# Kernel optimization log

Measured on AMD Instinct MI355X. Metric: run time of the kernel, lower is better.

The kernel has to match this reference:

```python
import jax, jax.numpy as jnp
import numpy as np

NH = 8    # num_heads
HD = 64   # head_dim
EPS = 1e-6


def setup_inputs() -> dict:
    key = jax.random.key(0)
    ks = jax.random.split(key, 8)
    B, N, D = 16, 3136, 512
    x = jax.random.normal(ks[0], (B, N, D), jnp.float32)
    Wq = jax.random.normal(ks[1], (D, D), jnp.float32) * 0.02
    Wkv = jax.random.normal(ks[2], (D, 2 * D), jnp.float32) * 0.02
    pos_enc = jax.random.normal(ks[3], (1, N, D), jnp.float32) * 0.02
    # depthwise conv: fan_out = k*k*out/groups = 25
    dwc_w = jax.random.normal(ks[4], (HD, 1, 5, 5), jnp.float32) * np.sqrt(2.0 / 25.0).astype(np.float32)
    dwc_b = jnp.zeros((HD,), jnp.float32)
    Wp = jax.random.normal(ks[5], (D, D), jnp.float32) * 0.02
    bp = jnp.zeros((D,), jnp.float32)
    return {"x": x, "Wq": Wq, "Wkv": Wkv, "pos_enc": pos_enc,
            "dwc_w": dwc_w, "dwc_b": dwc_b, "Wp": Wp, "bp": bp,
            "H": 56, "W": 56}


def reference(x, Wq, Wkv, pos_enc, dwc_w, dwc_b, Wp, bp, H, W):
    B, N, D = x.shape
    # projections (qkv_bias=False)
    q = jax.nn.relu(x @ Wq)                       # ReLU feature map on q
    kv = x @ Wkv                                  # [B, N, 2D]
    k = jax.nn.relu(kv[..., :D] + pos_enc)        # pos enc added before ReLU kernel
    v = kv[..., D:]
    # split heads: b n (h c) -> b h n c
    qh = q.reshape(B, N, NH, HD).transpose(0, 2, 1, 3)
    kh = k.reshape(B, N, NH, HD).transpose(0, 2, 1, 3)
    vh = v.reshape(B, N, NH, HD).transpose(0, 2, 1, 3)
    # linear attention: normalization and KV context
    k_sum = kh.sum(axis=2)                                        # [B, NH, HD]
    d_inv = 1.0 / (jnp.einsum('bhnd,bhd->bhn', qh, k_sum) + EPS)  # [B, NH, N]
    ctx = jnp.einsum('bhmd,bhme->bhde', kh, vh)                   # [B, NH, HD, HD]
    attn = jnp.einsum('bhnd,bhde->bhne', qh, ctx) * d_inv[..., None]
    # depthwise conv positional mixing on v (N == H*W)
    fmap = vh.reshape(B * NH, H, W, HD).transpose(0, 3, 1, 2)     # [(b h), c, H, W]
    dwc = jax.lax.conv_general_dilated(
        fmap, dwc_w, window_strides=(1, 1), padding='SAME',
        feature_group_count=HD,
        dimension_numbers=('NCHW', 'OIHW', 'NCHW')) + dwc_b[None, :, None, None]
    dwc = dwc.transpose(0, 2, 3, 1).reshape(B, NH, N, HD)
    # NOTE: original torch code reshapes ((b h), n, c) -> (B, N, D) directly
    # (NOT the inverse rearrange); reproduce that exact flat reshape.
    out = (attn + dwc).reshape(B, N, D)
    return out @ Wp + bp
```

## Files before the change

### kernel.cpp

```cpp
#include <hip/hip_runtime.h>

__device__ __forceinline__ float b2f(ushort u) {
    union { float f; unsigned int i; } w; w.i = ((unsigned int)u) << 16; return w.f;
}
__device__ __forceinline__ ushort f2b(float f) {
    union { float f; unsigned int i; } w; w.f = f;
    unsigned int lsb = (w.i >> 16) & 1u;
    w.i += 0x7fffu + lsb;
    return (ushort)(w.i >> 16);
}

typedef __bf16 bf16x8 __attribute__((ext_vector_type(8)));
typedef float floatx4 __attribute__((ext_vector_type(4)));

__device__ __forceinline__ void async_copy16(ushort* lds_base, const ushort* gptr) {
    __builtin_amdgcn_global_load_lds(
        (const __attribute__((address_space(1))) unsigned int*)gptr,
        (__attribute__((address_space(3))) unsigned int*)lds_base,
        16, 0, 0);
}

#define BATCH 16
#define NTOK  3136
#define NHEAD 8
#define HDIM  64
#define HSP   56
#define MROWS (BATCH * NTOK)
#define KDIM  512

__global__ __launch_bounds__(256) void detect_dtype(const ushort* __restrict__ x,
                                                    int* __restrict__ flag)
{
    __shared__ int s;
    if (threadIdx.x == 0) s = 0;
    __syncthreads();
    int bad = 0;
    for (int i = threadIdx.x; i < 4096; i += 256) {
        int e = (x[i] >> 7) & 0xFF;
        if (e >= 0x90) bad = 1;
    }
    if (bad) s = 1;
    __syncthreads();
    if (threadIdx.x == 0) flag[0] = s;
}

__global__ __launch_bounds__(256) void convert_x(
    const void* __restrict__ x, const int* __restrict__ flag,
    ushort* __restrict__ xbf)
{
    size_t t = (size_t)blockIdx.x * 256 + threadIdx.x;
    if (flag[0]) {
        const float* xf = (const float*)x + t * 8;
        float4 f0 = *(const float4*)xf;
        float4 f1 = *(const float4*)(xf + 4);
        ushort o[8] = { f2b(f0.x), f2b(f0.y), f2b(f0.z), f2b(f0.w),
                        f2b(f1.x), f2b(f1.y), f2b(f1.z), f2b(f1.w) };
        *(uint4*)(xbf + t * 8) = *(const uint4*)o;
    } else {
        *(uint4*)(xbf + t * 8) = *((const uint4*)x + t);
    }
}

__global__ __launch_bounds__(256) void prep_weights(
    const void* __restrict__ Wq, const void* __restrict__ Wkv,
    const void* __restrict__ Wp, const int* __restrict__ flag,
    ushort* __restrict__ WqkvT, ushort* __restrict__ WpT)
{
    bool f32 = flag[0] != 0;
    int idx = blockIdx.x * 256 + threadIdx.x;
    int kk = idx & 511;
    int n  = idx >> 9;
    if (n < 1536) {
        ushort val;
        if (n < 512)
            val = f32 ? f2b(((const float*)Wq)[kk * 512 + n])
                      : ((const ushort*)Wq)[kk * 512 + n];
        else
            val = f32 ? f2b(((const float*)Wkv)[kk * 1024 + (n - 512)])
                      : ((const ushort*)Wkv)[kk * 1024 + (n - 512)];
        WqkvT[n * 512 + kk] = val;
    } else {
        int n2 = n - 1536;
        WpT[n2 * 512 + kk] = f32 ? f2b(((const float*)Wp)[kk * 512 + n2])
                                 : ((const ushort*)Wp)[kk * 512 + n2];
    }
}

__global__ __launch_bounds__(256) void prep_dwc(
    const void* __restrict__ dwc_w, const void* __restrict__ dwc_b,
    const int* __restrict__ flag, float* __restrict__ wT)
{
    bool f32 = flag[0] != 0;
    for (int i = threadIdx.x; i < 1600; i += 256) {
        int e = i / 25, tap = i % 25;
        float w = f32 ? ((const float*)dwc_w)[i] : b2f(((const ushort*)dwc_w)[i]);
        wT[tap * 64 + e] = w;
    }
    if (threadIdx.x < 64) {
        float b = f32 ? ((const float*)dwc_b)[threadIdx.x]
                      : b2f(((const ushort*)dwc_b)[threadIdx.x]);
        wT[1600 + threadIdx.x] = b;
    }
}

__device__ __forceinline__ int swz(int r) { return (r ^ (r >> 2)) & 3; }

#define VMWAIT(N) asm volatile("s_waitcnt vmcnt(" #N ")" ::: "memory")
#define LGKM0()   do { asm volatile("s_waitcnt lgkmcnt(0)" ::: "memory"); \
                       __builtin_amdgcn_sched_barrier(0); } while (0)
#define ASLOT(u,h) ((((u) & 1) * 2 + (h)) * 8192)
#define BSLOT(u,h) (32768 + (((u) & 1) * 2 + (h)) * 8192)

__global__ __launch_bounds__(512, 2) void gemm256_bt(
    const ushort* __restrict__ A, const ushort* __restrict__ Bt,
    int mode, const int* __restrict__ flag,
    const void* __restrict__ pos_enc, const void* __restrict__ bias,
    void* __restrict__ out0, ushort* __restrict__ out1, ushort* __restrict__ out2,
    int ntn)
{
    __shared__ ushort smem[65536];

    const bool f32 = flag[0] != 0;
    const int tid = threadIdx.x;
    const int lam = tid & 63;
    const int w   = tid >> 6;
    const int wm  = w >> 2;
    const int wn  = w & 3;
    const int g    = lam >> 4;
    const int mrow = lam & 15;

    const int nwg = gridDim.x;
    const int q8  = nwg >> 3;
    const int bid = blockIdx.x;
    const int fid = (bid & 7) * q8 + (bid >> 3);
    const int tm = fid / ntn, tn = fid - tm * ntn;
    const int m0 = tm * 256, n0 = tn * 256;

    const int srow  = w * 16 + (lam >> 3);
    const int scol8 = 8 * ((lam & 7) ^ (lam >> 3));
    const ushort* gA0 = A  + (size_t)(m0 +       srow) * KDIM + scol8;
    const ushort* gA1 = A  + (size_t)(m0 + 128 + srow) * KDIM + scol8;
    const ushort* gB0 = Bt + (size_t)(n0 +       srow) * KDIM + scol8;
    const ushort* gB1 = Bt + (size_t)(n0 + 128 + srow) * KDIM + scol8;

    const int m7  = mrow & 7;
    const int kx0 = 8 * (g ^ m7);
    const int kx1 = 8 * ((4 + g) ^ m7);
    const int aRow = mrow * 64;
    const int bRow = ((wn & 1) * 64 + mrow) * 64;

    floatx4 acc[8][4];
    #pragma unroll
    for (int i = 0; i < 8; i++)
        #pragma unroll
        for (int j = 0; j < 4; j++) acc[i][j] = (floatx4)0.f;

#define STG(gp, sb, ko) do { \
    async_copy16(smem + (sb) + w * 1024,       (gp) + (ko)); \
    async_copy16(smem + (sb) + w * 1024 + 512, (gp) + 4096 + (ko)); } while (0)

    STG(gA0, ASLOT(0,0), 0);  STG(gA1, ASLOT(0,1), 0);
    STG(gB0, BSLOT(0,0), 0);  STG(gB1, BSLOT(0,1), 0);
    STG(gA0, ASLOT(1,0), 64); STG(gA1, ASLOT(1,1), 64);
    STG(gB0, BSLOT(1,0), 64); STG(gB1, BSLOT(1,1), 64);
    VMWAIT(8);
    __builtin_amdgcn_s_barrier();

    bf16x8 a[2][2], bb[4][2];

#define PHASE_MFMA(P) do { \
    __builtin_amdgcn_s_setprio(1); \
    _Pragma("unroll") \
    for (int q = 0; q < 2; ++q) \
        _Pragma("unroll") \
        for (int fc = 0; fc < 4; ++fc) { \
            acc[2*(P)+q][fc] = __builtin_amdgcn_mfma_f32_16x16x32_bf16( \
                bb[fc][0], a[q][0], acc[2*(P)+q][fc], 0, 0, 0); \
            acc[2*(P)+q][fc] = __builtin_amdgcn_mfma_f32_16x16x32_bf16( \
                bb[fc][1], a[q][1], acc[2*(P)+q][fc], 0, 0, 0); \
        } \
    __builtin_amdgcn_s_setprio(0); } while (0)

    #pragma unroll
    for (int u = 0; u < 8; ++u) {
        const ushort* sa = smem + ASLOT(u, wm) + aRow;
        const ushort* sb = smem + BSLOT(u, (wn >> 1)) + bRow;

        #pragma unroll
        for (int q = 0; q < 2; ++q) {
            a[q][0] = *(const bf16x8*)(sa + q * 1024 + kx0);
            a[q][1] = *(const bf16x8*)(sa + q * 1024 + kx1);
        }
        #pragma unroll
        for (int fc = 0; fc < 4; ++fc) {
            bb[fc][0] = *(const bf16x8*)(sb + fc * 1024 + kx0);
            bb[fc][1] = *(const bf16x8*)(sb + fc * 1024 + kx1);
        }
        if (u >= 1 && u <= 6) STG(gA0, ASLOT(u + 1, 0), (u + 1) * 64);
        __builtin_amdgcn_s_barrier();
        LGKM0();
        PHASE_MFMA(0);
        __builtin_amdgcn_s_barrier();

        #pragma unroll
        for (int q = 0; q < 2; ++q) {
            a[q][0] = *(const bf16x8*)(sa + (2 + q) * 1024 + kx0);
            a[q][1] = *(const bf16x8*)(sa + (2 + q) * 1024 + kx1);
        }
        if (u >= 1 && u <= 6) STG(gA1, ASLOT(u + 1, 1), (u + 1) * 64);
        if (u <= 5)           STG(gB0, BSLOT(u + 2, 0), (u + 2) * 64);
        __builtin_amdgcn_s_barrier();
        LGKM0();
        PHASE_MFMA(1);
        __builtin_amdgcn_s_barrier();

        #pragma unroll
        for (int q = 0; q < 2; ++q) {
            a[q][0] = *(const bf16x8*)(sa + (4 + q) * 1024 + kx0);
            a[q][1] = *(const bf16x8*)(sa + (4 + q) * 1024 + kx1);
        }
        if (u <= 5) STG(gB1, BSLOT(u + 2, 1), (u + 2) * 64);
        __builtin_amdgcn_s_barrier();
        LGKM0();
        PHASE_MFMA(2);
        __builtin_amdgcn_s_barrier();

        #pragma unroll
        for (int q = 0; q < 2; ++q) {
            a[q][0] = *(const bf16x8*)(sa + (6 + q) * 1024 + kx0);
            a[q][1] = *(const bf16x8*)(sa + (6 + q) * 1024 + kx1);
        }
        __builtin_amdgcn_s_barrier();
        LGKM0();
        PHASE_MFMA(3);
        if (u <= 5)      VMWAIT(4);
        else if (u == 6) VMWAIT(0);
        if (u < 7) __builtin_amdgcn_s_barrier();
    }

    const int cb0 = n0 + wn * 64;
    #pragma unroll
    for (int fr = 0; fr < 8; ++fr) {
        const int rg  = m0 + wm * 128 + fr * 16 + mrow;
        const int bb2 = rg / NTOK;
        const int nn  = rg - bb2 * NTOK;
        if (mode == 1) {
            if (f32) {
                float* orow = (float*)out0 + (size_t)rg * 512 + cb0 + g * 4;
                #pragma unroll
                for (int fc = 0; fc < 4; ++fc) {
                    float ob[4];
                    #pragma unroll
                    for (int r = 0; r < 4; ++r)
                        ob[r] = acc[fr][fc][r] +
                                ((const float*)bias)[cb0 + fc * 16 + g * 4 + r];
                    *(float4*)(orow + fc * 16) = *(const float4*)ob;
                }
            } else {
                ushort* orow = (ushort*)out0 + (size_t)rg * 512 + cb0 + g * 4;
                #pragma unroll
                for (int fc = 0; fc < 4; ++fc) {
                    ushort t4[4];
                    #pragma unroll
                    for (int r = 0; r < 4; ++r)
                        t4[r] = f2b(acc[fr][fc][r] +
                                    b2f(((const ushort*)bias)[cb0 + fc * 16 + g * 4 + r]));
                    *(uint2*)(orow + fc * 16) = *(const uint2*)t4;
                }
            }
        } else {
            const int tz   = cb0 >> 9;
            const int head = (cb0 >> 6) & 7;
            const size_t obase =
                (((size_t)bb2 * 8 + head) * NTOK + nn) * 64 + g * 4;
            if (tz == 0) {
                #pragma unroll
                for (int fc = 0; fc < 4; ++fc) {
                    ushort t4[4];
                    #pragma unroll
                    for (int r = 0; r < 4; ++r)
                        t4[r] = f2b(fmaxf(acc[fr][fc][r], 0.f));
                    *(uint2*)((ushort*)out0 + obase + fc * 16) = *(const uint2*)t4;
                }
            } else if (tz == 1) {
                const int d0 = cb0 - 512 + g * 4;
                #pragma unroll
                for (int fc = 0; fc < 4; ++fc) {
                    ushort t4[4];
                    #pragma unroll
                    for (int r = 0; r < 4; ++r) {
                        float pe = f32
                            ? ((const float*)pos_enc)[(size_t)nn * 512 + d0 + fc * 16 + r]
                            : b2f(((const ushort*)pos_enc)[(size_t)nn * 512 + d0 + fc * 16 + r]);
                        t4[r] = f2b(fmaxf(acc[fr][fc][r] + pe, 0.f));
                    }
                    *(uint2*)(out1 + obase + fc * 16) = *(const uint2*)t4;
                }
            } else {
                #pragma unroll
                for (int fc = 0; fc < 4; ++fc) {
                    ushort t4[4];
                    #pragma unroll
                    for (int r = 0; r < 4; ++r)
                        t4[r] = f2b(acc[fr][fc][r]);
                    *(uint2*)(out2 + obase + fc * 16) = *(const uint2*)t4;
                }
            }
        }
    }
#undef STG
#undef PHASE_MFMA
}

#define SPLITS 7
#define NPER   (NTOK / SPLITS)

__global__ __launch_bounds__(256) void ctx_ksum(
    const ushort* __restrict__ kbuf, const ushort* __restrict__ vbuf,
    float* __restrict__ ctx, float* __restrict__ ksum)
{
    __shared__ ushort kT[64 * 32];
    __shared__ ushort vT[64 * 32];
    __shared__ float ks4[256];
    int bh = blockIdx.x, sp = blockIdx.y;
    int tid = threadIdx.x;
    int lane = tid & 63, wave = tid >> 6;
    int mrow = lane & 15, g = lane >> 4;
    int r = tid & 31, cblk = tid >> 5;
    size_t base = ((size_t)bh * NTOK + sp * NPER) * 64;

    floatx4 acc[4];
    #pragma unroll
    for (int c = 0; c < 4; c++) acc[c] = (floatx4)0.f;
    float kpart = 0.f;
    int kd = tid >> 2, kq = tid & 3;

    for (int nc = 0; nc < NPER; nc += 32) {
        uint4 ku = *(const uint4*)(kbuf + base + (size_t)(nc + r) * 64 + cblk * 8);
        uint4 vu = *(const uint4*)(vbuf + base + (size_t)(nc + r) * 64 + cblk * 8);
        __syncthreads();
        const ushort* kp = (const ushort*)&ku;
        const ushort* vp = (const ushort*)&vu;
        #pragma unroll
        for (int j = 0; j < 8; j++) {
            int d = cblk * 8 + j;
            int blk = (r >> 3) ^ swz(d);
            kT[d * 32 + blk * 8 + (r & 7)] = kp[j];
            vT[d * 32 + blk * 8 + (r & 7)] = vp[j];
        }
        __syncthreads();
        {
            const ushort* p = &kT[kd * 32 + kq * 8];
            #pragma unroll
            for (int j = 0; j < 8; j++) kpart += b2f(p[j]);
        }
        int dr = wave * 16 + mrow;
        bf16x8 af = *(const bf16x8*)&kT[dr * 32 + (g ^ swz(dr)) * 8];
        #pragma unroll
        for (int c = 0; c < 4; c++) {
            int er = c * 16 + mrow;
            bf16x8 bf = *(const bf16x8*)&vT[er * 32 + (g ^ swz(er)) * 8];
            acc[c] = __builtin_amdgcn_mfma_f32_16x16x32_bf16(af, bf, acc[c], 0, 0, 0);
        }
    }
    #pragma unroll
    for (int c = 0; c < 4; c++)
        #pragma unroll
        for (int rr = 0; rr < 4; rr++) {
            int d = wave * 16 + g * 4 + rr;
            int e = c * 16 + mrow;
            atomicAdd(&ctx[bh * 4096 + d * 64 + e], acc[c][rr]);
        }
    ks4[tid] = kpart;
    __syncthreads();
    if (tid < 64) {
        float s = ks4[tid * 4] + ks4[tid * 4 + 1] + ks4[tid * 4 + 2] + ks4[tid * 4 + 3];
        atomicAdd(&ksum[bh * 64 + tid], s);
    }
}

__global__ __launch_bounds__(256) void attn_kernel(
    const ushort* __restrict__ q, const float* __restrict__ ctx,
    const float* __restrict__ ksum, ushort* __restrict__ ybuf)
{
    __shared__ float smem[4352];
    ushort* ctxT = (ushort*)smem;
    float* sout = smem;
    int bh = blockIdx.x, cg = blockIdx.y;
    int tid = threadIdx.x;
    int lane = tid & 63, wave = tid >> 6;
    int mrow = lane & 15, g = lane >> 4;

    for (int i = tid; i < 640; i += 256) {
        int e = i >> 3, blk = i & 7;
        ushort tmp[8];
        #pragma unroll
        for (int j = 0; j < 8; j++) {
            int d = blk * 8 + j;
            float v = 0.f;
            if (e < 64) v = ctx[bh * 4096 + d * 64 + e];
            else if (e == 64) v = ksum[bh * 64 + d];
            tmp[j] = f2b(v);
        }
        *(uint4*)&ctxT[e * 64 + (blk ^ (e & 7)) * 8] = *(const uint4*)tmp;
    }
    __syncthreads();

    bf16x8 bfr[2][5];
    #pragma unroll
    for (int kt = 0; kt < 2; kt++)
        #pragma unroll
        for (int c = 0; c < 5; c++) {
            int e = c * 16 + mrow;
            bfr[kt][c] = *(const bf16x8*)&ctxT[e * 64 + ((kt * 4 + g) ^ (e & 7)) * 8];
        }

    int token4 = tid >> 2, seg = tid & 3;
    for (int cc = 0; cc < 7; cc++) {
        int n0 = (cg * 7 + cc) * 64;
        floatx4 acc[5];
        #pragma unroll
        for (int c = 0; c < 5; c++) acc[c] = (floatx4)0.f;
        size_t qrow = ((size_t)bh * NTOK + n0 + wave * 16 + mrow) * 64;
        #pragma unroll
        for (int kt = 0; kt < 2; kt++) {
            bf16x8 af = *(const bf16x8*)(q + qrow + kt * 32 + g * 8);
            #pragma unroll
            for (int c = 0; c < 5; c++)
                acc[c] = __builtin_amdgcn_mfma_f32_16x16x32_bf16(af, bfr[kt][c], acc[c], 0, 0, 0);
        }
        __syncthreads();
        #pragma unroll
        for (int c = 0; c < 4; c++)
            #pragma unroll
            for (int rr = 0; rr < 4; rr++)
                sout[(wave * 16 + g * 4 + rr) * 68 + c * 16 + mrow] = acc[c][rr];
        if (mrow == 0) {
            #pragma unroll
            for (int rr = 0; rr < 4; rr++)
                sout[(wave * 16 + g * 4 + rr) * 68 + 64] = acc[4][rr];
        }
        __syncthreads();
        float dinv = 1.0f / (sout[token4 * 68 + 64] + 1e-6f);
        const float* sp = &sout[token4 * 68 + seg * 16];
        ushort res[16];
        #pragma unroll
        for (int j = 0; j < 16; j++) res[j] = f2b(sp[j] * dinv);
        ushort* o = ybuf + ((size_t)bh * NTOK + n0 + token4) * 64 + seg * 16;
        *(uint4*)o = *(const uint4*)res;
        *(uint4*)(o + 8) = *(const uint4*)(res + 8);
    }
}

__global__ __launch_bounds__(256) void dwc_add(
    const ushort* __restrict__ v, const float* __restrict__ wT,
    ushort* __restrict__ ybuf)
{
    __shared__ float wls[1664];
    for (int i = threadIdx.x; i < 1664; i += 256) wls[i] = wT[i];
    __syncthreads();

    int t = blockIdx.x * 256 + threadIdx.x;
    int eg = (t & 7) * 8;
    int r = t >> 3;
    int n  = r % NTOK;
    int bh = r / NTOK;
    int y = n / HSP, x = n % HSP;

    float acc[8];
    #pragma unroll
    for (int j = 0; j < 8; j++) acc[j] = wls[1600 + eg + j];

    const ushort* vb = v + (size_t)bh * NTOK * 64 + eg;
    #pragma unroll
    for (int dy = 0; dy < 5; ++dy) {
        int yy = y + dy - 2;
        if (yy < 0 || yy >= HSP) continue;
        #pragma unroll
        for (int dx = 0; dx < 5; ++dx) {
            int xx = x + dx - 2;
            if (xx < 0 || xx >= HSP) continue;
            uint4 u = *(const uint4*)(vb + (size_t)(yy * HSP + xx) * 64);
            const ushort* up = (const ushort*)&u;
            const float* wp = &wls[(dy * 5 + dx) * 64 + eg];
            #pragma unroll
            for (int j = 0; j < 8; j++) acc[j] += wp[j] * b2f(up[j]);
        }
    }
    size_t o = (size_t)r * 64 + eg;
    uint4 yo = *(const uint4*)(ybuf + o);
    const ushort* yp = (const ushort*)&yo;
    ushort res[8];
    #pragma unroll
    for (int j = 0; j < 8; j++) res[j] = f2b(acc[j] + b2f(yp[j]));
    *(uint4*)(ybuf + o) = *(const uint4*)res;
}

extern "C" void kernel_launch(void* const* d_in, const int* in_sizes, int n_in,
                              void* d_out, int out_size, void* d_ws, size_t ws_size,
                              hipStream_t stream) {
    const void* x    = d_in[0];
    const void* Wq   = d_in[1];
    const void* Wkv  = d_in[2];
    const void* pos  = d_in[3];
    const void* dwcw = d_in[4];
    const void* dwcb = d_in[5];
    const void* Wp   = d_in[6];
    const void* bp   = d_in[7];

    char* ws = (char*)d_ws;
    const size_t SZ_BIG = 51380224;
    int*    flag   = (int*)(ws + 0);
    ushort* WqkvT  = (ushort*)(ws + 4096);
    ushort* WpT    = (ushort*)(ws + 4096 + 1572864);
    float*  wTdwc  = (float*)(ws + 2101248);
    float*  ctx    = (float*)(ws + 2107904);
    float*  ksum   = (float*)(ws + 4205056);
    ushort* qbuf   = (ushort*)(ws + 4237824);
    ushort* kbuf   = (ushort*)(ws + 4237824 + SZ_BIG);
    ushort* vbuf   = (ushort*)(ws + 4237824 + 2 * SZ_BIG);
    ushort* xbf = (ushort*)d_out;

    detect_dtype<<<1, 256, 0, stream>>>((const ushort*)x, flag);
    hipMemsetAsync(ctx, 0, 2097152 + 32768, stream);

    prep_weights<<<4096, 256, 0, stream>>>(Wq, Wkv, Wp, flag, WqkvT, WpT);
    prep_dwc<<<1, 256, 0, stream>>>(dwcw, dwcb, flag, wTdwc);
    convert_x<<<12544, 256, 0, stream>>>(x, flag, xbf);

    gemm256_bt<<<dim3(196 * 6), 512, 0, stream>>>(
        xbf, WqkvT, 0, flag, pos, nullptr, qbuf, kbuf, vbuf, 6);

    ctx_ksum<<<dim3(128, SPLITS), 256, 0, stream>>>(kbuf, vbuf, ctx, ksum);

    attn_kernel<<<dim3(128, 7), 256, 0, stream>>>(qbuf, ctx, ksum, kbuf);

    dwc_add<<<12544, 256, 0, stream>>>(vbuf, wTdwc, kbuf);

    gemm256_bt<<<dim3(196 * 2), 512, 0, stream>>>(
        kbuf, WpT, 1, flag, nullptr, bp, d_out, nullptr, nullptr, 2);
}
```

Before: 537.0 us.

## Restructure GEMM to 128x256 tiles with 4 waves and triple-buffered K=32 stages

The bf16 GEMM kernel moves from 256x256 tiles with 8 waves and double-buffered K=64 stages to 128x256 tiles with 4 waves, K=32 steps and a three-slot LDS ring. The barriers between phases inside each stage are gone, leaving one barrier per K step. Each wave now computes a 64x128 sub-tile with 4x8 MFMAs per step, and the grid doubles. The aim is more blocks per CU (less LDS per block) and better latency hiding, at the cost of less operand reuse per tile and more K iterations.

```diff
diff --git a/kernel.cpp b/kernel.cpp
--- a/kernel.cpp
+++ b/kernel.cpp
@@ -108,24 +108,24 @@
 #define VMWAIT(N) asm volatile("s_waitcnt vmcnt(" #N ")" ::: "memory")
 #define LGKM0()   do { asm volatile("s_waitcnt lgkmcnt(0)" ::: "memory"); \
                        __builtin_amdgcn_sched_barrier(0); } while (0)
-#define ASLOT(u,h) ((((u) & 1) * 2 + (h)) * 8192)
-#define BSLOT(u,h) (32768 + (((u) & 1) * 2 + (h)) * 8192)
-
-__global__ __launch_bounds__(512, 2) void gemm256_bt(
+#define ASLOT(u) (((u) % 3) * 4096)
+#define BSLOT(u) (12288 + ((u) % 3) * 8192)
+
+__global__ __launch_bounds__(256, 2) void gemm256_bt(
     const ushort* __restrict__ A, const ushort* __restrict__ Bt,
     int mode, const int* __restrict__ flag,
     const void* __restrict__ pos_enc, const void* __restrict__ bias,
     void* __restrict__ out0, ushort* __restrict__ out1, ushort* __restrict__ out2,
     int ntn)
 {
-    __shared__ ushort smem[65536];
+    __shared__ ushort smem[36864];
 
     const bool f32 = flag[0] != 0;
     const int tid = threadIdx.x;
     const int lam = tid & 63;
     const int w   = tid >> 6;
-    const int wm  = w >> 2;
-    const int wn  = w & 3;
+    const int wm  = w >> 1;
+    const int wn  = w & 1;
     const int g    = lam >> 4;
     const int mrow = lam & 15;
 
@@ -134,121 +134,77 @@
     const int bid = blockIdx.x;
     const int fid = (bid & 7) * q8 + (bid >> 3);
     const int tm = fid / ntn, tn = fid - tm * ntn;
-    const int m0 = tm * 256, n0 = tn * 256;
-
-    const int srow  = w * 16 + (lam >> 3);
-    const int scol8 = 8 * ((lam & 7) ^ (lam >> 3));
-    const ushort* gA0 = A  + (size_t)(m0 +       srow) * KDIM + scol8;
-    const ushort* gA1 = A  + (size_t)(m0 + 128 + srow) * KDIM + scol8;
-    const ushort* gB0 = Bt + (size_t)(n0 +       srow) * KDIM + scol8;
-    const ushort* gB1 = Bt + (size_t)(n0 + 128 + srow) * KDIM + scol8;
-
-    const int m7  = mrow & 7;
-    const int kx0 = 8 * (g ^ m7);
-    const int kx1 = 8 * ((4 + g) ^ m7);
-    const int aRow = mrow * 64;
-    const int bRow = ((wn & 1) * 64 + mrow) * 64;
-
-    floatx4 acc[8][4];
-    #pragma unroll
-    for (int i = 0; i < 8; i++)
-        #pragma unroll
-        for (int j = 0; j < 4; j++) acc[i][j] = (floatx4)0.f;
-
-#define STG(gp, sb, ko) do { \
-    async_copy16(smem + (sb) + w * 1024,       (gp) + (ko)); \
-    async_copy16(smem + (sb) + w * 1024 + 512, (gp) + 4096 + (ko)); } while (0)
-
-    STG(gA0, ASLOT(0,0), 0);  STG(gA1, ASLOT(0,1), 0);
-    STG(gB0, BSLOT(0,0), 0);  STG(gB1, BSLOT(0,1), 0);
-    STG(gA0, ASLOT(1,0), 64); STG(gA1, ASLOT(1,1), 64);
-    STG(gB0, BSLOT(1,0), 64); STG(gB1, BSLOT(1,1), 64);
-    VMWAIT(8);
+    const int m0 = tm * 128, n0 = tn * 256;
+
+    const int scol8 = 8 * ((lam & 3) ^ ((lam >> 3) & 3));
+    const int srowA = w * 32 + (lam >> 2);
+    const int srowB = w * 64 + (lam >> 2);
+    const ushort* gA = A  + (size_t)(m0 + srowA) * KDIM + scol8;
+    const ushort* gB = Bt + (size_t)(n0 + srowB) * KDIM + scol8;
+
+    const int axor  = (g ^ ((mrow >> 1) & 3)) << 3;
+    const int aBase = (wm * 64 + mrow) * 32 + axor;
+    const int bBase = (wn * 128 + mrow) * 32 + axor;
+
+    floatx4 acc[4][8];
+    #pragma unroll
+    for (int i = 0; i < 4; i++)
+        #pragma unroll
+        for (int j = 0; j < 8; j++) acc[i][j] = (floatx4)0.f;
+
+#define STGA(u) do { \
+    async_copy16(smem + ASLOT(u) + w * 1024,       gA + (u) * 32); \
+    async_copy16(smem + ASLOT(u) + w * 1024 + 512, gA + 16 * KDIM + (u) * 32); } while (0)
+#define STGB(u) do { \
+    async_copy16(smem + BSLOT(u) + w * 2048,        gB + (u) * 32); \
+    async_copy16(smem + BSLOT(u) + w * 2048 + 512,  gB + 16 * KDIM + (u) * 32); \
+    async_copy16(smem + BSLOT(u) + w * 2048 + 1024, gB + 32 * KDIM + (u) * 32); \
+    async_copy16(smem + BSLOT(u) + w * 2048 + 1536, gB + 48 * KDIM + (u) * 32); } while (0)
+
+    STGA(0); STGB(0);
+    STGA(1); STGB(1);
+    VMWAIT(6);
     __builtin_amdgcn_s_barrier();
 
-    bf16x8 a[2][2], bb[4][2];
-
-#define PHASE_MFMA(P) do { \
-    __builtin_amdgcn_s_setprio(1); \
-    _Pragma("unroll") \
-    for (int q = 0; q < 2; ++q) \
-        _Pragma("unroll") \
-        for (int fc = 0; fc < 4; ++fc) { \
-            acc[2*(P)+q][fc] = __builtin_amdgcn_mfma_f32_16x16x32_bf16( \
-                bb[fc][0], a[q][0], acc[2*(P)+q][fc], 0, 0, 0); \
-            acc[2*(P)+q][fc] = __builtin_amdgcn_mfma_f32_16x16x32_bf16( \
-                bb[fc][1], a[q][1], acc[2*(P)+q][fc], 0, 0, 0); \
-        } \
-    __builtin_amdgcn_s_setprio(0); } while (0)
-
-    #pragma unroll
-    for (int u = 0; u < 8; ++u) {
-        const ushort* sa = smem + ASLOT(u, wm) + aRow;
-        const ushort* sb = smem + BSLOT(u, (wn >> 1)) + bRow;
-
-        #pragma unroll
-        for (int q = 0; q < 2; ++q) {
-            a[q][0] = *(const bf16x8*)(sa + q * 1024 + kx0);
-            a[q][1] = *(const bf16x8*)(sa + q * 1024 + kx1);
-        }
-        #pragma unroll
-        for (int fc = 0; fc < 4; ++fc) {
-            bb[fc][0] = *(const bf16x8*)(sb + fc * 1024 + kx0);
-            bb[fc][1] = *(const bf16x8*)(sb + fc * 1024 + kx1);
-        }
-        if (u >= 1 && u <= 6) STG(gA0, ASLOT(u + 1, 0), (u + 1) * 64);
-        __builtin_amdgcn_s_barrier();
+    #pragma unroll
+    for (int u = 0; u < 16; ++u) {
+        if (u <= 13) { STGA(u + 2); STGB(u + 2); }
+
+        const ushort* sa = smem + ASLOT(u) + aBase;
+        const ushort* sb = smem + BSLOT(u) + bBase;
+        bf16x8 a[4], bfr[8];
+        #pragma unroll
+        for (int fr = 0; fr < 4; ++fr) a[fr] = *(const bf16x8*)(sa + fr * 512);
+        #pragma unroll
+        for (int fc = 0; fc < 8; ++fc) bfr[fc] = *(const bf16x8*)(sb + fc * 512);
         LGKM0();
-        PHASE_MFMA(0);
-        __builtin_amdgcn_s_barrier();
-
-        #pragma unroll
-        for (int q = 0; q < 2; ++q) {
-            a[q][0] = *(const bf16x8*)(sa + (2 + q) * 1024 + kx0);
-            a[q][1] = *(const bf16x8*)(sa + (2 + q) * 1024 + kx1);
-        }
-        if (u >= 1 && u <= 6) STG(gA1, ASLOT(u + 1, 1), (u + 1) * 64);
-        if (u <= 5)           STG(gB0, BSLOT(u + 2, 0), (u + 2) * 64);
-        __builtin_amdgcn_s_barrier();
-        LGKM0();
-        PHASE_MFMA(1);
-        __builtin_amdgcn_s_barrier();
-
-        #pragma unroll
-        for (int q = 0; q < 2; ++q) {
-            a[q][0] = *(const bf16x8*)(sa + (4 + q) * 1024 + kx0);
-            a[q][1] = *(const bf16x8*)(sa + (4 + q) * 1024 + kx1);
-        }
-        if (u <= 5) STG(gB1, BSLOT(u + 2, 1), (u + 2) * 64);
-        __builtin_amdgcn_s_barrier();
-        LGKM0();
-        PHASE_MFMA(2);
-        __builtin_amdgcn_s_barrier();
-
-        #pragma unroll
-        for (int q = 0; q < 2; ++q) {
-            a[q][0] = *(const bf16x8*)(sa + (6 + q) * 1024 + kx0);
-            a[q][1] = *(const bf16x8*)(sa + (6 + q) * 1024 + kx1);
-        }
-        __builtin_amdgcn_s_barrier();
-        LGKM0();
-        PHASE_MFMA(3);
-        if (u <= 5)      VMWAIT(4);
-        else if (u == 6) VMWAIT(0);
-        if (u < 7) __builtin_amdgcn_s_barrier();
-    }
-
-    const int cb0 = n0 + wn * 64;
-    #pragma unroll
-    for (int fr = 0; fr < 8; ++fr) {
-        const int rg  = m0 + wm * 128 + fr * 16 + mrow;
+
+        __builtin_amdgcn_s_setprio(1);
+        #pragma unroll
+        for (int fr = 0; fr < 4; ++fr)
+            #pragma unroll
+            for (int fc = 0; fc < 8; ++fc)
+                acc[fr][fc] = __builtin_amdgcn_mfma_f32_16x16x32_bf16(
+                    bfr[fc], a[fr], acc[fr][fc], 0, 0, 0);
+        __builtin_amdgcn_s_setprio(0);
+
+        if (u <= 13)      VMWAIT(6);
+        else if (u == 14) VMWAIT(0);
+        if (u < 15) __builtin_amdgcn_s_barrier();
+    }
+
+    const int cb0 = n0 + wn * 128;
+    const int tz  = cb0 >> 9;
+    #pragma unroll
+    for (int fr = 0; fr < 4; ++fr) {
+        const int rg  = m0 + wm * 64 + fr * 16 + mrow;
         const int bb2 = rg / NTOK;
         const int nn  = rg - bb2 * NTOK;
         if (mode == 1) {
             if (f32) {
                 float* orow = (float*)out0 + (size_t)rg * 512 + cb0 + g * 4;
                 #pragma unroll
-                for (int fc = 0; fc < 4; ++fc) {
+                for (int fc = 0; fc < 8; ++fc) {
                     float ob[4];
                     #pragma unroll
                     for (int r = 0; r < 4; ++r)
@@ -259,7 +215,7 @@
             } else {
                 ushort* orow = (ushort*)out0 + (size_t)rg * 512 + cb0 + g * 4;
                 #pragma unroll
-                for (int fc = 0; fc < 4; ++fc) {
+                for (int fc = 0; fc < 8; ++fc) {
                     ushort t4[4];
                     #pragma unroll
                     for (int r = 0; r < 4; ++r)
@@ -269,47 +225,39 @@
                 }
             }
         } else {
-            const int tz   = cb0 >> 9;
-            const int head = (cb0 >> 6) & 7;
-            const size_t obase =
-                (((size_t)bb2 * 8 + head) * NTOK + nn) * 64 + g * 4;
-            if (tz == 0) {
-                #pragma unroll
-                for (int fc = 0; fc < 4; ++fc) {
-                    ushort t4[4];
+            #pragma unroll
+            for (int fc = 0; fc < 8; ++fc) {
+                const int colg = cb0 + fc * 16 + g * 4;
+                const int head = (colg >> 6) & 7;
+                const size_t obase =
+                    (((size_t)bb2 * 8 + head) * NTOK + nn) * 64 + (colg & 63);
+                ushort t4[4];
+                if (tz == 0) {
                     #pragma unroll
                     for (int r = 0; r < 4; ++r)
                         t4[r] = f2b(fmaxf(acc[fr][fc][r], 0.f));
-                    *(uint2*)((ushort*)out0 + obase + fc * 16) = *(const uint2*)t4;
-                }
-            } else if (tz == 1) {
-                const int d0 = cb0 - 512 + g * 4;
-                #pragma unroll
-                for (int fc = 0; fc < 4; ++fc) {
-                    ushort t4[4];
+                    *(uint2*)((ushort*)out0 + obase) = *(const uint2*)t4;
+                } else if (tz == 1) {
+                    const int d0 = colg - 512;
                     #pragma unroll
                     for (int r = 0; r < 4; ++r) {
                         float pe = f32
-                            ? ((const float*)pos_enc)[(size_t)nn * 512 + d0 + fc * 16 + r]
-                            : b2f(((const ushort*)pos_enc)[(size_t)nn * 512 + d0 + fc * 16 + r]);
+                            ? ((const float*)pos_enc)[(size_t)nn * 512 + d0 + r]
+                            : b2f(((const ushort*)pos_enc)[(size_t)nn * 512 + d0 + r]);
                         t4[r] = f2b(fmaxf(acc[fr][fc][r] + pe, 0.f));
                     }
-                    *(uint2*)(out1 + obase + fc * 16) = *(const uint2*)t4;
-                }
-            } else {
-                #pragma unroll
-                for (int fc = 0; fc < 4; ++fc) {
-                    ushort t4[4];
+                    *(uint2*)(out1 + obase) = *(const uint2*)t4;
+                } else {
                     #pragma unroll
                     for (int r = 0; r < 4; ++r)
                         t4[r] = f2b(acc[fr][fc][r]);
-                    *(uint2*)(out2 + obase + fc * 16) = *(const uint2*)t4;
+                    *(uint2*)(out2 + obase) = *(const uint2*)t4;
                 }
             }
         }
     }
-#undef STG
-#undef PHASE_MFMA
+#undef STGA
+#undef STGB
 }
 
 #define SPLITS 7
@@ -528,7 +476,7 @@
     prep_dwc<<<1, 256, 0, stream>>>(dwcw, dwcb, flag, wTdwc);
     convert_x<<<12544, 256, 0, stream>>>(x, flag, xbf);
 
-    gemm256_bt<<<dim3(196 * 6), 512, 0, stream>>>(
+    gemm256_bt<<<dim3(392 * 6), 256, 0, stream>>>(
         xbf, WqkvT, 0, flag, pos, nullptr, qbuf, kbuf, vbuf, 6);
 
     ctx_ksum<<<dim3(128, SPLITS), 256, 0, stream>>>(kbuf, vbuf, ctx, ksum);
@@ -537,6 +485,6 @@
 
     dwc_add<<<12544, 256, 0, stream>>>(vbuf, wTdwc, kbuf);
 
-    gemm256_bt<<<dim3(196 * 2), 512, 0, stream>>>(
+    gemm256_bt<<<dim3(392 * 2), 256, 0, stream>>>(
         kbuf, WpT, 1, flag, nullptr, bp, d_out, nullptr, nullptr, 2);
 }
```

New measurement: 546.3 us. Within noise of the previous version (+1.7%).
